# Kernel optimization log

Hardware: AMD Instinct MI355X
Metric: run time of the kernel (lower is better)

The kernel has to match this reference:

```python
import jax, jax.numpy as jnp
import numpy as np

# HalfKA_v2 canonical constants
FT_INPUT_DIM = 45056
FT_OUTPUT_DIM = 1024
PSQT_BUCKETS = 8
LAYER_STACKS = 8
FC0_OUT = 16
L2 = 15
FC1_IN_PAD = 32
FC1_OUT = 32
FC2_IN_PAD = 32
B = 8192
FEATS = 32  # active features per sample


def round_ste(x):
    # forward: round; backward: identity (straight-through)
    return x + jax.lax.stop_gradient(jnp.round(x) - x)


def fake_quant(w, bits):
    qmax = (1 << (bits - 1)) - 1
    return jnp.clip(round_ste(w), -qmax - 1, qmax)


def sparse_sum(w, feats, offsets, nb):
    # EmbeddingBag(mode='sum'): gather rows and segment-sum per sample.
    gathered = w[feats]                               # [total_feats, D]
    n = feats.shape[0]
    sid = jnp.zeros((n,), jnp.int32).at[offsets[1:]].set(1).cumsum()
    return jax.ops.segment_sum(gathered, sid, num_segments=nb)


def setup_inputs() -> dict:
    key = jax.random.key(0)
    ks = jax.random.split(key, 8)
    w_feats = jax.random.randint(ks[0], (B * FEATS,), 0, FT_INPUT_DIM)
    b_feats = jax.random.randint(ks[1], (B * FEATS,), 0, FT_INPUT_DIM)
    offs = jnp.arange(B, dtype=jnp.int32) * FEATS
    stm = jax.random.randint(ks[2], (B,), 0, 2)
    bucket = jax.random.randint(ks[3], (B,), 0, LAYER_STACKS)
    ft_weight = jax.random.normal(ks[4], (FT_INPUT_DIM, FT_OUTPUT_DIM), jnp.float32) * 5.0
    ft_bias = jnp.full((FT_OUTPUT_DIM,), 30.0, jnp.float32)
    psqt_weight = jnp.zeros((FT_INPUT_DIM, PSQT_BUCKETS), jnp.float32)
    fc0_w = jax.random.normal(ks[5], (LAYER_STACKS, FC0_OUT, FT_OUTPUT_DIM), jnp.float32) * 3.0
    fc0_b = jnp.zeros((LAYER_STACKS, FC0_OUT), jnp.float32)
    fc1_w = jax.random.normal(ks[6], (LAYER_STACKS, FC1_OUT, FC1_IN_PAD), jnp.float32) * 3.0
    fc1_b = jnp.zeros((LAYER_STACKS, FC1_OUT), jnp.float32)
    fc2_w = jax.random.normal(ks[7], (LAYER_STACKS, 1, FC2_IN_PAD), jnp.float32) * 3.0
    fc2_b = jnp.zeros((LAYER_STACKS, 1), jnp.float32)
    return dict(w_feats=w_feats, w_offsets=offs, b_feats=b_feats, b_offsets=offs,
                stm=stm, bucket=bucket, ft_weight=ft_weight, ft_bias=ft_bias,
                psqt_weight=psqt_weight, fc0_w=fc0_w, fc0_b=fc0_b,
                fc1_w=fc1_w, fc1_b=fc1_b, fc2_w=fc2_w, fc2_b=fc2_b)


def reference(w_feats, w_offsets, b_feats, b_offsets, stm, bucket,
              ft_weight, ft_bias, psqt_weight,
              fc0_w, fc0_b, fc1_w, fc1_b, fc2_w, fc2_b):
    nb = stm.shape[0]
    ftw = fake_quant(ft_weight, 16)
    ftb = fake_quant(ft_bias, 16)
    psq = fake_quant(psqt_weight, 32)

    acc_w = sparse_sum(ftw, w_feats, w_offsets, nb) + ftb
    acc_b = sparse_sum(ftw, b_feats, b_offsets, nb) + ftb
    psqt_w = sparse_sum(psq, w_feats, w_offsets, nb)
    psqt_b = sparse_sum(psq, b_feats, b_offsets, nb)

    stm_f = stm.astype(ft_weight.dtype)[:, None]
    acc_stm = acc_w * (1 - stm_f) + acc_b * stm_f
    acc_opp = acc_b * (1 - stm_f) + acc_w * stm_f

    H = FT_OUTPUT_DIM // 2

    def pairwise(a):
        return jnp.clip(a[:, :H], 0.0, 127.0) * jnp.clip(a[:, H:], 0.0, 127.0) / 128.0

    ft = jnp.concatenate([pairwise(acc_stm), pairwise(acc_opp)], axis=-1)  # [B, 1024]

    fc0w = fake_quant(fc0_w, 8); fc0b = fake_quant(fc0_b, 32)
    fc1w = fake_quant(fc1_w, 8); fc1b = fake_quant(fc1_b, 32)
    fc2w = fake_quant(fc2_w, 8); fc2b = fake_quant(fc2_b, 32)

    bsel3 = bucket[:, None, None]
    # fc0: compute all 8 tiny stacks, then select per-sample bucket (equivalent to mask routing)
    o0_all = jnp.einsum('bf,sof->bso', ft, fc0w) + fc0b[None]      # [B, S, 16]
    o0 = jnp.take_along_axis(o0_all, bsel3, axis=1)[:, 0]           # [B, 16]

    sqr = jnp.clip(o0[:, :L2] ** 2 / float(1 << 19), 0.0, 127.0)
    rel = jnp.clip(o0[:, :L2] / float(1 << 6), 0.0, 127.0)
    slab = jnp.concatenate([sqr, rel, jnp.zeros((nb, FC1_IN_PAD - 2 * L2), ft.dtype)], axis=-1)

    o1_all = jnp.einsum('bi,soi->bso', slab, fc1w) + fc1b[None]     # [B, S, 32]
    o1 = jnp.take_along_axis(o1_all, bsel3, axis=1)[:, 0]
    ac1 = jnp.clip(o1 / float(1 << 6), 0.0, 127.0)

    o2_all = jnp.einsum('bi,soi->bso', ac1, fc2w) + fc2b[None]      # [B, S, 1]
    scalar = jnp.take_along_axis(o2_all, bsel3, axis=1)[:, 0]       # [B, 1]

    skip = o0[:, 15:16] * (9600.0 / 8128.0)
    positional = scalar + skip

    psqt_stm = psqt_w * (1 - stm_f) + psqt_b * stm_f
    psqt_opp = psqt_b * (1 - stm_f) + psqt_w * stm_f
    bsel = bucket[:, None]
    psqt_v = (jnp.take_along_axis(psqt_stm, bsel, axis=1)
              - jnp.take_along_axis(psqt_opp, bsel, axis=1)) / 2.0

    return ((psqt_v + positional)[:, 0]) / 16.0
```

## Files before the change

kernel.cpp:

```cpp
#include <hip/hip_runtime.h>


#define NFEATS 32
#define FT_OUT 1024
#define HALF   512
#define NC4    256
#define TBL_BYTES  (45056u * 1024u)
#define TBL_N4     11534336
#define FC0Q_BYTES (8u * 16u * 1024u * 4u)

typedef short v2s __attribute__((ext_vector_type(2)));

__device__ __forceinline__ float q16f(float x) {
    float r = rintf(x);
    return fminf(fmaxf(r, -32768.f), 32767.f);
}
__device__ __forceinline__ float q8f(float x) {
    float r = rintf(x);
    return fminf(fmaxf(r, -128.f), 127.f);
}
__device__ __forceinline__ float4 q8f4(float4 v) {
    return make_float4(q8f(v.x), q8f(v.y), q8f(v.z), q8f(v.w));
}
__device__ __forceinline__ float clip127(float x) {
    return fminf(fmaxf(x, 0.f), 127.f);
}

__device__ __forceinline__ v2s sx_even(int p) {
    union { int i; v2s s; } u; u.i = p << 8; u.s = u.s >> 8; return u.s;
}
__device__ __forceinline__ v2s sx_odd(int p) {
    union { int i; v2s s; } u; u.i = p; u.s = u.s >> 8; return u.s;
}

__device__ __forceinline__ int pack4i8(float4 v) {
    const int a = (int)rintf(fminf(fmaxf(v.x, -127.f), 127.f));
    const int b = (int)rintf(fminf(fmaxf(v.y, -127.f), 127.f));
    const int c = (int)rintf(fminf(fmaxf(v.z, -127.f), 127.f));
    const int d = (int)rintf(fminf(fmaxf(v.w, -127.f), 127.f));
    return (a & 0xff) | ((b & 0xff) << 8) | ((c & 0xff) << 16) | (d << 24);
}

__global__ __launch_bounds__(256) void cvt_all(
    const float4* __restrict__ tbl, int* __restrict__ tbl_o,
    const float4* __restrict__ fc0, float4* __restrict__ fc0_o,
    int tbl_n4, int fc0_n4)
{
    const int i = blockIdx.x * 256 + threadIdx.x;
    if (i < tbl_n4) {
        tbl_o[i] = pack4i8(tbl[i]);
    } else {
        const int j = i - tbl_n4;
        if (j < fc0_n4) fc0_o[j] = q8f4(fc0[j]);
    }
}

template <int MODE>
__global__ __launch_bounds__(256) void nnue_v2(
    const int* __restrict__ w_feats, const int* __restrict__ w_offsets,
    const int* __restrict__ b_feats, const int* __restrict__ b_offsets,
    const int* __restrict__ stm_arr, const int* __restrict__ bucket_arr,
    const float* __restrict__ ft_weight, const char* __restrict__ ft_i8,
    const float* __restrict__ ft_bias,
    const float* __restrict__ psqt_weight,
    const float* __restrict__ fc0_w, const float* __restrict__ wq0,
    const float* __restrict__ fc0_b,
    const float* __restrict__ fc1_w, const float* __restrict__ fc1_b,
    const float* __restrict__ fc2_w, const float* __restrict__ fc2_b,
    float* __restrict__ out,
    int n_wf, int n_bf, int nb)
{
    const int b = blockIdx.x;
    const int t = threadIdx.x;
    const int l = t & 63;
    const int w = t >> 6;

    __shared__ int   s_fw[NFEATS], s_fb[NFEATS];
    __shared__ v2s   s_part[2][4][512];
    __shared__ float s_stm[FT_OUT];
    __shared__ float s_opp[FT_OUT];
    __shared__ float s_ft[FT_OUT];
    __shared__ float s_o0[16];
    __shared__ float s_slab[32];
    __shared__ float s_ac1[32];
    __shared__ float s_psqt[2];

    const int ws = w_offsets[b];
    const int we = (b + 1 < nb) ? w_offsets[b + 1] : n_wf;
    const int bs = b_offsets[b];
    const int be = (b + 1 < nb) ? b_offsets[b + 1] : n_bf;
    const int cw = min(we - ws, NFEATS);
    const int cb = min(be - bs, NFEATS);

    if (t < NFEATS) {
        s_fw[t] = (t < cw) ? w_feats[ws + t] : 0;
    } else if (t < 2 * NFEATS) {
        const int k = t - NFEATS;
        s_fb[k] = (k < cb) ? b_feats[bs + k] : 0;
    }
    __syncthreads();

    const int stm = stm_arr[b];
    const int bk  = bucket_arr[b];

    if (t < 64) {
        const int side = t >> 5;
        const int k    = t & 31;
        const int cnt  = side ? cb : cw;
        float v = 0.f;
        if (k < cnt) {
            const int f = side ? s_fb[k] : s_fw[k];
            v = rintf(psqt_weight[f * 8 + bk]);
        }
        v += __shfl_down(v, 16, 32);
        v += __shfl_down(v,  8, 32);
        v += __shfl_down(v,  4, 32);
        v += __shfl_down(v,  2, 32);
        v += __shfl_down(v,  1, 32);
        if (k == 0) s_psqt[side] = v;
    }

    float4 fw4, fb4;

    if constexpr (MODE >= 1) {
        v2s eW[4] = {{0,0},{0,0},{0,0},{0,0}}, oW[4] = {{0,0},{0,0},{0,0},{0,0}};
        v2s eB[4] = {{0,0},{0,0},{0,0},{0,0}}, oB[4] = {{0,0},{0,0},{0,0},{0,0}};
        const char* bp = ft_i8 + (size_t)(l * 16);

        if (cw == NFEATS && cb == NFEATS) {
            #pragma unroll
            for (int i = 0; i < 8; ++i) {
                const int k = w + 4 * i;
                const int4 p = *(const int4*)(bp + (size_t)s_fw[k] * 1024);
                const int4 q = *(const int4*)(bp + (size_t)s_fb[k] * 1024);
                eW[0] += sx_even(p.x); oW[0] += sx_odd(p.x);
                eW[1] += sx_even(p.y); oW[1] += sx_odd(p.y);
                eW[2] += sx_even(p.z); oW[2] += sx_odd(p.z);
                eW[3] += sx_even(p.w); oW[3] += sx_odd(p.w);
                eB[0] += sx_even(q.x); oB[0] += sx_odd(q.x);
                eB[1] += sx_even(q.y); oB[1] += sx_odd(q.y);
                eB[2] += sx_even(q.z); oB[2] += sx_odd(q.z);
                eB[3] += sx_even(q.w); oB[3] += sx_odd(q.w);
            }
        } else {
            for (int k = w; k < cw; k += 4) {
                const int4 p = *(const int4*)(bp + (size_t)s_fw[k] * 1024);
                eW[0] += sx_even(p.x); oW[0] += sx_odd(p.x);
                eW[1] += sx_even(p.y); oW[1] += sx_odd(p.y);
                eW[2] += sx_even(p.z); oW[2] += sx_odd(p.z);
                eW[3] += sx_even(p.w); oW[3] += sx_odd(p.w);
            }
            for (int k = w; k < cb; k += 4) {
                const int4 q = *(const int4*)(bp + (size_t)s_fb[k] * 1024);
                eB[0] += sx_even(q.x); oB[0] += sx_odd(q.x);
                eB[1] += sx_even(q.y); oB[1] += sx_odd(q.y);
                eB[2] += sx_even(q.z); oB[2] += sx_odd(q.z);
                eB[3] += sx_even(q.w); oB[3] += sx_odd(q.w);
            }
        }

        #pragma unroll
        for (int d = 0; d < 4; ++d) {
            s_part[0][w][d * 128 + 2 * l    ] = eW[d];
            s_part[0][w][d * 128 + 2 * l + 1] = oW[d];
            s_part[1][w][d * 128 + 2 * l    ] = eB[d];
            s_part[1][w][d * 128 + 2 * l + 1] = oB[d];
        }
        __syncthreads();

        const int ri = (t & 3) * 128 + 2 * (t >> 2);
        v2s ew = s_part[0][0][ri];     ew += s_part[0][1][ri];
        ew += s_part[0][2][ri];        ew += s_part[0][3][ri];
        v2s ow = s_part[0][0][ri + 1]; ow += s_part[0][1][ri + 1];
        ow += s_part[0][2][ri + 1];    ow += s_part[0][3][ri + 1];
        v2s eb = s_part[1][0][ri];     eb += s_part[1][1][ri];
        eb += s_part[1][2][ri];        eb += s_part[1][3][ri];
        v2s ob = s_part[1][0][ri + 1]; ob += s_part[1][1][ri + 1];
        ob += s_part[1][2][ri + 1];    ob += s_part[1][3][ri + 1];
        fw4 = make_float4((float)ew.x, (float)ow.x, (float)ew.y, (float)ow.y);
        fb4 = make_float4((float)eb.x, (float)ob.x, (float)eb.y, (float)ob.y);
    } else {
        const float4* ftw4 = reinterpret_cast<const float4*>(ft_weight);
        float4 aw = make_float4(0.f, 0.f, 0.f, 0.f);
        float4 ab = make_float4(0.f, 0.f, 0.f, 0.f);
        for (int k = 0; k < cw; ++k) {
            const float4 v = ftw4[s_fw[k] * NC4 + t];
            aw.x += rintf(v.x); aw.y += rintf(v.y);
            aw.z += rintf(v.z); aw.w += rintf(v.w);
        }
        for (int k = 0; k < cb; ++k) {
            const float4 u = ftw4[s_fb[k] * NC4 + t];
            ab.x += rintf(u.x); ab.y += rintf(u.y);
            ab.z += rintf(u.z); ab.w += rintf(u.w);
        }
        fw4 = aw; fb4 = ab;
    }

    {
        const float4 bv = reinterpret_cast<const float4*>(ft_bias)[t];
        const float bx = q16f(bv.x), by = q16f(bv.y), bz = q16f(bv.z), bw = q16f(bv.w);
        fw4.x += bx; fw4.y += by; fw4.z += bz; fw4.w += bw;
        fb4.x += bx; fb4.y += by; fb4.z += bz; fb4.w += bw;
    }

    reinterpret_cast<float4*>(s_stm)[t] = stm ? fb4 : fw4;
    reinterpret_cast<float4*>(s_opp)[t] = stm ? fw4 : fb4;
    __syncthreads();

    {
        float4 lo, hi;
        if (t < 128) {
            lo = reinterpret_cast<const float4*>(s_stm)[t];
            hi = reinterpret_cast<const float4*>(s_stm)[t + 128];
        } else {
            lo = reinterpret_cast<const float4*>(s_opp)[t - 128];
            hi = reinterpret_cast<const float4*>(s_opp)[t];
        }
        float4 r;
        r.x = clip127(lo.x) * clip127(hi.x) * 0.0078125f;
        r.y = clip127(lo.y) * clip127(hi.y) * 0.0078125f;
        r.z = clip127(lo.z) * clip127(hi.z) * 0.0078125f;
        r.w = clip127(lo.w) * clip127(hi.w) * 0.0078125f;
        reinterpret_cast<float4*>(s_ft)[t] = r;
    }
    __syncthreads();

    {
        const float4* ftf4 = reinterpret_cast<const float4*>(s_ft);
        const float4 f0 = ftf4[l], f1 = ftf4[l + 64],
                     f2 = ftf4[l + 128], f3 = ftf4[l + 192];
        const float4* wbase = (MODE == 2)
            ? reinterpret_cast<const float4*>(wq0)
            : reinterpret_cast<const float4*>(fc0_w);
        #pragma unroll
        for (int o = 0; o < 4; ++o) {
            const int orow = 4 * w + o;
            const float4* wr = wbase + ((size_t)bk * 16 + orow) * NC4;
            float4 w0 = wr[l], w1 = wr[l + 64], w2 = wr[l + 128], w3 = wr[l + 192];
            if constexpr (MODE != 2) {
                w0 = q8f4(w0); w1 = q8f4(w1); w2 = q8f4(w2); w3 = q8f4(w3);
            }
            float acc = f0.x * w0.x + f0.y * w0.y + f0.z * w0.z + f0.w * w0.w
                      + f1.x * w1.x + f1.y * w1.y + f1.z * w1.z + f1.w * w1.w
                      + f2.x * w2.x + f2.y * w2.y + f2.z * w2.z + f2.w * w2.w
                      + f3.x * w3.x + f3.y * w3.y + f3.z * w3.z + f3.w * w3.w;
            acc += __shfl_down(acc, 32);
            acc += __shfl_down(acc, 16);
            acc += __shfl_down(acc,  8);
            acc += __shfl_down(acc,  4);
            acc += __shfl_down(acc,  2);
            acc += __shfl_down(acc,  1);
            if (l == 0) s_o0[orow] = acc + rintf(fc0_b[bk * 16 + orow]);
        }
    }
    __syncthreads();

    if (t < 32) {
        float v;
        if (t < 15) {
            const float x = s_o0[t];
            v = clip127(x * x * (1.f / 524288.f));
        } else if (t < 30) {
            v = clip127(s_o0[t - 15] * 0.015625f);
        } else {
            v = 0.f;
        }
        s_slab[t] = v;
    }
    __syncthreads();

    if (t < 32) {
        const float* w1 = fc1_w + (size_t)bk * 32 * 32 + t * 32;
        float acc = rintf(fc1_b[bk * 32 + t]);
        #pragma unroll
        for (int i = 0; i < 32; ++i)
            acc += s_slab[i] * q8f(w1[i]);
        s_ac1[t] = clip127(acc * 0.015625f);
    }
    __syncthreads();

    if (t == 0) {
        const float* w2 = fc2_w + (size_t)bk * 32;
        float acc = rintf(fc2_b[bk]);
        #pragma unroll
        for (int i = 0; i < 32; ++i)
            acc += s_ac1[i] * q8f(w2[i]);
        const float skip = s_o0[15] * (float)(9600.0 / 8128.0);
        const float ps   = stm ? s_psqt[1] : s_psqt[0];
        const float po   = stm ? s_psqt[0] : s_psqt[1];
        out[b] = (0.5f * (ps - po) + acc + skip) * 0.0625f;
    }
}

extern "C" void kernel_launch(void* const* d_in, const int* in_sizes, int n_in,
                              void* d_out, int out_size, void* d_ws, size_t ws_size,
                              hipStream_t stream) {
    const int*   w_feats   = (const int*)d_in[0];
    const int*   w_offsets = (const int*)d_in[1];
    const int*   b_feats   = (const int*)d_in[2];
    const int*   b_offsets = (const int*)d_in[3];
    const int*   stm       = (const int*)d_in[4];
    const int*   bucket    = (const int*)d_in[5];
    const float* ft_weight = (const float*)d_in[6];
    const float* ft_bias   = (const float*)d_in[7];
    const float* psqt_w    = (const float*)d_in[8];
    const float* fc0_w     = (const float*)d_in[9];
    const float* fc0_b     = (const float*)d_in[10];
    const float* fc1_w     = (const float*)d_in[11];
    const float* fc1_b     = (const float*)d_in[12];
    const float* fc2_w     = (const float*)d_in[13];
    const float* fc2_b     = (const float*)d_in[14];
    float*       out       = (float*)d_out;

    const int nb   = in_sizes[4];
    const int n_wf = in_sizes[0];
    const int n_bf = in_sizes[2];

    const bool has_i8 = ws_size >= TBL_BYTES;
    const bool has_wq = ws_size >= TBL_BYTES + FC0Q_BYTES;
    float* wq0 = (float*)((char*)d_ws + TBL_BYTES);

    if (has_i8) {
        const int fc0_n4 = has_wq ? 32768 : 0;
        const int nblk = (TBL_N4 + fc0_n4 + 255) / 256;
        cvt_all<<<nblk, 256, 0, stream>>>(
            (const float4*)ft_weight, (int*)d_ws,
            (const float4*)fc0_w, (float4*)wq0, TBL_N4, fc0_n4);
        if (has_wq) {
            nnue_v2<2><<<nb, 256, 0, stream>>>(
                w_feats, w_offsets, b_feats, b_offsets, stm, bucket,
                ft_weight, (const char*)d_ws, ft_bias, psqt_w,
                fc0_w, wq0, fc0_b, fc1_w, fc1_b, fc2_w, fc2_b,
                out, n_wf, n_bf, nb);
        } else {
            nnue_v2<1><<<nb, 256, 0, stream>>>(
                w_feats, w_offsets, b_feats, b_offsets, stm, bucket,
                ft_weight, (const char*)d_ws, ft_bias, psqt_w,
                fc0_w, nullptr, fc0_b, fc1_w, fc1_b, fc2_w, fc2_b,
                out, n_wf, n_bf, nb);
        }
    } else {
        nnue_v2<0><<<nb, 256, 0, stream>>>(
            w_feats, w_offsets, b_feats, b_offsets, stm, bucket,
            ft_weight, nullptr, ft_bias, psqt_w,
            fc0_w, nullptr, fc0_b, fc1_w, fc1_b, fc2_w, fc2_b,
            out, n_wf, n_bf, nb);
    }
}
```

Measured before the change: 391.2 us.

## Split feature-transformer gather by side and drop cross-wave partial reduction

The sparse gather changes so each half of the block (128 threads) handles one perspective: every thread reads 8 bytes per row across all 32 features, instead of four waves each taking a quarter of the features and reducing partials through shared memory. This removes the s_part shared buffer, one barrier and the reduction pass, and shrinks LDS use. In exchange each thread issues more serial dependent loads. The conversion kernel now packs 8 float4s per thread, and the fc1 and fc2 weights are also pre-quantized into the workspace.

```diff
diff --git a/kernel.cpp b/kernel.cpp
--- a/kernel.cpp
+++ b/kernel.cpp
@@ -3,11 +3,14 @@
 
 #define NFEATS 32
 #define FT_OUT 1024
-#define HALF   512
 #define NC4    256
 #define TBL_BYTES  (45056u * 1024u)
 #define TBL_N4     11534336
-#define FC0Q_BYTES (8u * 16u * 1024u * 4u)
+#define TBL_G8     (TBL_N4 / 8)
+#define FC0_N4     32768
+#define FC1_N4     2048
+#define FC2_N4     64
+#define WQ_BYTES   ((FC0_N4 + FC1_N4 + FC2_N4) * 16u)
 
 typedef short v2s __attribute__((ext_vector_type(2)));
 
@@ -25,7 +28,6 @@
 __device__ __forceinline__ float clip127(float x) {
     return fminf(fmaxf(x, 0.f), 127.f);
 }
-
 __device__ __forceinline__ v2s sx_even(int p) {
     union { int i; v2s s; } u; u.i = p << 8; u.s = u.s >> 8; return u.s;
 }
@@ -41,29 +43,41 @@
     return (a & 0xff) | ((b & 0xff) << 8) | ((c & 0xff) << 16) | (d << 24);
 }
 
-__global__ __launch_bounds__(256) void cvt_all(
-    const float4* __restrict__ tbl, int* __restrict__ tbl_o,
-    const float4* __restrict__ fc0, float4* __restrict__ fc0_o,
-    int tbl_n4, int fc0_n4)
+__global__ __launch_bounds__(256) void cvt_v3(
+    const float4* __restrict__ tbl, int4* __restrict__ tbl_o,
+    const float4* __restrict__ fc0, const float4* __restrict__ fc1,
+    const float4* __restrict__ fc2, float4* __restrict__ wq,
+    int do_fc)
 {
     const int i = blockIdx.x * 256 + threadIdx.x;
-    if (i < tbl_n4) {
-        tbl_o[i] = pack4i8(tbl[i]);
-    } else {
-        const int j = i - tbl_n4;
-        if (j < fc0_n4) fc0_o[j] = q8f4(fc0[j]);
+    if (i < TBL_G8) {
+        const float4* p = tbl + (size_t)i * 8;
+        int4 a, b;
+        a.x = pack4i8(p[0]); a.y = pack4i8(p[1]);
+        a.z = pack4i8(p[2]); a.w = pack4i8(p[3]);
+        b.x = pack4i8(p[4]); b.y = pack4i8(p[5]);
+        b.z = pack4i8(p[6]); b.w = pack4i8(p[7]);
+        tbl_o[2 * (size_t)i]     = a;
+        tbl_o[2 * (size_t)i + 1] = b;
+    } else if (do_fc) {
+        int j = i - TBL_G8;
+        if (j < FC0_N4) { wq[j] = q8f4(fc0[j]); return; }
+        j -= FC0_N4;
+        if (j < FC1_N4) { wq[FC0_N4 + j] = q8f4(fc1[j]); return; }
+        j -= FC1_N4;
+        if (j < FC2_N4) { wq[FC0_N4 + FC1_N4 + j] = q8f4(fc2[j]); }
     }
 }
 
 template <int MODE>
-__global__ __launch_bounds__(256) void nnue_v2(
+__global__ __launch_bounds__(256) void nnue_v3(
     const int* __restrict__ w_feats, const int* __restrict__ w_offsets,
     const int* __restrict__ b_feats, const int* __restrict__ b_offsets,
     const int* __restrict__ stm_arr, const int* __restrict__ bucket_arr,
     const float* __restrict__ ft_weight, const char* __restrict__ ft_i8,
     const float* __restrict__ ft_bias,
     const float* __restrict__ psqt_weight,
-    const float* __restrict__ fc0_w, const float* __restrict__ wq0,
+    const float* __restrict__ fc0_w, const float* __restrict__ wq,
     const float* __restrict__ fc0_b,
     const float* __restrict__ fc1_w, const float* __restrict__ fc1_b,
     const float* __restrict__ fc2_w, const float* __restrict__ fc2_b,
@@ -75,11 +89,9 @@
     const int l = t & 63;
     const int w = t >> 6;
 
-    __shared__ int   s_fw[NFEATS], s_fb[NFEATS];
-    __shared__ v2s   s_part[2][4][512];
-    __shared__ float s_stm[FT_OUT];
-    __shared__ float s_opp[FT_OUT];
-    __shared__ float s_ft[FT_OUT];
+    __shared__ int s_fw[NFEATS], s_fb[NFEATS];
+    __shared__ __align__(16) float s_acc[2][FT_OUT];
+    __shared__ __align__(16) float s_ft[FT_OUT];
     __shared__ float s_o0[16];
     __shared__ float s_slab[32];
     __shared__ float s_ac1[32];
@@ -120,65 +132,38 @@
         if (k == 0) s_psqt[side] = v;
     }
 
-    float4 fw4, fb4;
-
     if constexpr (MODE >= 1) {
-        v2s eW[4] = {{0,0},{0,0},{0,0},{0,0}}, oW[4] = {{0,0},{0,0},{0,0},{0,0}};
-        v2s eB[4] = {{0,0},{0,0},{0,0},{0,0}}, oB[4] = {{0,0},{0,0},{0,0},{0,0}};
-        const char* bp = ft_i8 + (size_t)(l * 16);
-
+        const int side = t >> 7;
+        const int u    = t & 127;
+        const int* rows = side ? s_fb : s_fw;
+        const int  cnt  = side ? cb : cw;
+        const char* bp = ft_i8 + (size_t)(u * 8);
+
+        v2s e0 = {0,0}, o0 = {0,0}, e1 = {0,0}, o1 = {0,0};
         if (cw == NFEATS && cb == NFEATS) {
-            #pragma unroll
-            for (int i = 0; i < 8; ++i) {
-                const int k = w + 4 * i;
-                const int4 p = *(const int4*)(bp + (size_t)s_fw[k] * 1024);
-                const int4 q = *(const int4*)(bp + (size_t)s_fb[k] * 1024);
-                eW[0] += sx_even(p.x); oW[0] += sx_odd(p.x);
-                eW[1] += sx_even(p.y); oW[1] += sx_odd(p.y);
-                eW[2] += sx_even(p.z); oW[2] += sx_odd(p.z);
-                eW[3] += sx_even(p.w); oW[3] += sx_odd(p.w);
-                eB[0] += sx_even(q.x); oB[0] += sx_odd(q.x);
-                eB[1] += sx_even(q.y); oB[1] += sx_odd(q.y);
-                eB[2] += sx_even(q.z); oB[2] += sx_odd(q.z);
-                eB[3] += sx_even(q.w); oB[3] += sx_odd(q.w);
+            #pragma unroll 8
+            for (int k = 0; k < NFEATS; ++k) {
+                const int2 p = *(const int2*)(bp + (size_t)rows[k] * 1024);
+                e0 += sx_even(p.x); o0 += sx_odd(p.x);
+                e1 += sx_even(p.y); o1 += sx_odd(p.y);
             }
         } else {
-            for (int k = w; k < cw; k += 4) {
-                const int4 p = *(const int4*)(bp + (size_t)s_fw[k] * 1024);
-                eW[0] += sx_even(p.x); oW[0] += sx_odd(p.x);
-                eW[1] += sx_even(p.y); oW[1] += sx_odd(p.y);
-                eW[2] += sx_even(p.z); oW[2] += sx_odd(p.z);
-                eW[3] += sx_even(p.w); oW[3] += sx_odd(p.w);
+            for (int k = 0; k < cnt; ++k) {
+                const int2 p = *(const int2*)(bp + (size_t)rows[k] * 1024);
+                e0 += sx_even(p.x); o0 += sx_odd(p.x);
+                e1 += sx_even(p.y); o1 += sx_odd(p.y);
             }
-            for (int k = w; k < cb; k += 4) {
-                const int4 q = *(const int4*)(bp + (size_t)s_fb[k] * 1024);
-                eB[0] += sx_even(q.x); oB[0] += sx_odd(q.x);
-                eB[1] += sx_even(q.y); oB[1] += sx_odd(q.y);
-                eB[2] += sx_even(q.z); oB[2] += sx_odd(q.z);
-                eB[3] += sx_even(q.w); oB[3] += sx_odd(q.w);
-            }
-        }
-
-        #pragma unroll
-        for (int d = 0; d < 4; ++d) {
-            s_part[0][w][d * 128 + 2 * l    ] = eW[d];
-            s_part[0][w][d * 128 + 2 * l + 1] = oW[d];
-            s_part[1][w][d * 128 + 2 * l    ] = eB[d];
-            s_part[1][w][d * 128 + 2 * l + 1] = oB[d];
-        }
-        __syncthreads();
-
-        const int ri = (t & 3) * 128 + 2 * (t >> 2);
-        v2s ew = s_part[0][0][ri];     ew += s_part[0][1][ri];
-        ew += s_part[0][2][ri];        ew += s_part[0][3][ri];
-        v2s ow = s_part[0][0][ri + 1]; ow += s_part[0][1][ri + 1];
-        ow += s_part[0][2][ri + 1];    ow += s_part[0][3][ri + 1];
-        v2s eb = s_part[1][0][ri];     eb += s_part[1][1][ri];
-        eb += s_part[1][2][ri];        eb += s_part[1][3][ri];
-        v2s ob = s_part[1][0][ri + 1]; ob += s_part[1][1][ri + 1];
-        ob += s_part[1][2][ri + 1];    ob += s_part[1][3][ri + 1];
-        fw4 = make_float4((float)ew.x, (float)ow.x, (float)ew.y, (float)ow.y);
-        fb4 = make_float4((float)eb.x, (float)ob.x, (float)eb.y, (float)ob.y);
+        }
+
+        const float4 b0 = reinterpret_cast<const float4*>(ft_bias)[2 * u];
+        const float4 b1 = reinterpret_cast<const float4*>(ft_bias)[2 * u + 1];
+        float4 r0, r1;
+        r0.x = (float)e0.x + q16f(b0.x); r0.y = (float)o0.x + q16f(b0.y);
+        r0.z = (float)e0.y + q16f(b0.z); r0.w = (float)o0.y + q16f(b0.w);
+        r1.x = (float)e1.x + q16f(b1.x); r1.y = (float)o1.x + q16f(b1.y);
+        r1.z = (float)e1.y + q16f(b1.z); r1.w = (float)o1.y + q16f(b1.w);
+        reinterpret_cast<float4*>(&s_acc[side][8 * u])[0] = r0;
+        reinterpret_cast<float4*>(&s_acc[side][8 * u])[1] = r1;
     } else {
         const float4* ftw4 = reinterpret_cast<const float4*>(ft_weight);
         float4 aw = make_float4(0.f, 0.f, 0.f, 0.f);
@@ -189,32 +174,29 @@
             aw.z += rintf(v.z); aw.w += rintf(v.w);
         }
         for (int k = 0; k < cb; ++k) {
-            const float4 u = ftw4[s_fb[k] * NC4 + t];
-            ab.x += rintf(u.x); ab.y += rintf(u.y);
-            ab.z += rintf(u.z); ab.w += rintf(u.w);
-        }
-        fw4 = aw; fb4 = ab;
-    }
-
-    {
+            const float4 u4 = ftw4[s_fb[k] * NC4 + t];
+            ab.x += rintf(u4.x); ab.y += rintf(u4.y);
+            ab.z += rintf(u4.z); ab.w += rintf(u4.w);
+        }
         const float4 bv = reinterpret_cast<const float4*>(ft_bias)[t];
         const float bx = q16f(bv.x), by = q16f(bv.y), bz = q16f(bv.z), bw = q16f(bv.w);
-        fw4.x += bx; fw4.y += by; fw4.z += bz; fw4.w += bw;
-        fb4.x += bx; fb4.y += by; fb4.z += bz; fb4.w += bw;
-    }
-
-    reinterpret_cast<float4*>(s_stm)[t] = stm ? fb4 : fw4;
-    reinterpret_cast<float4*>(s_opp)[t] = stm ? fw4 : fb4;
+        aw.x += bx; aw.y += by; aw.z += bz; aw.w += bw;
+        ab.x += bx; ab.y += by; ab.z += bz; ab.w += bw;
+        reinterpret_cast<float4*>(&s_acc[0][4 * t])[0] = aw;
+        reinterpret_cast<float4*>(&s_acc[1][4 * t])[0] = ab;
+    }
     __syncthreads();
 
     {
         float4 lo, hi;
         if (t < 128) {
-            lo = reinterpret_cast<const float4*>(s_stm)[t];
-            hi = reinterpret_cast<const float4*>(s_stm)[t + 128];
+            const float* sp = s_acc[stm];
+            lo = reinterpret_cast<const float4*>(sp)[t];
+            hi = reinterpret_cast<const float4*>(sp)[t + 128];
         } else {
-            lo = reinterpret_cast<const float4*>(s_opp)[t - 128];
-            hi = reinterpret_cast<const float4*>(s_opp)[t];
+            const float* sp = s_acc[1 - stm];
+            lo = reinterpret_cast<const float4*>(sp)[t - 128];
+            hi = reinterpret_cast<const float4*>(sp)[t];
         }
         float4 r;
         r.x = clip127(lo.x) * clip127(hi.x) * 0.0078125f;
@@ -230,7 +212,7 @@
         const float4 f0 = ftf4[l], f1 = ftf4[l + 64],
                      f2 = ftf4[l + 128], f3 = ftf4[l + 192];
         const float4* wbase = (MODE == 2)
-            ? reinterpret_cast<const float4*>(wq0)
+            ? reinterpret_cast<const float4*>(wq)
             : reinterpret_cast<const float4*>(fc0_w);
         #pragma unroll
         for (int o = 0; o < 4; ++o) {
@@ -270,21 +252,29 @@
     __syncthreads();
 
     if (t < 32) {
-        const float* w1 = fc1_w + (size_t)bk * 32 * 32 + t * 32;
+        const float* w1 = (MODE == 2)
+            ? wq + FC0_N4 * 4 + (size_t)bk * 32 * 32 + t * 32
+            : fc1_w + (size_t)bk * 32 * 32 + t * 32;
         float acc = rintf(fc1_b[bk * 32 + t]);
         #pragma unroll
-        for (int i = 0; i < 32; ++i)
-            acc += s_slab[i] * q8f(w1[i]);
+        for (int i = 0; i < 32; ++i) {
+            const float wv = (MODE == 2) ? w1[i] : q8f(w1[i]);
+            acc += s_slab[i] * wv;
+        }
         s_ac1[t] = clip127(acc * 0.015625f);
     }
     __syncthreads();
 
     if (t == 0) {
-        const float* w2 = fc2_w + (size_t)bk * 32;
+        const float* w2 = (MODE == 2)
+            ? wq + (FC0_N4 + FC1_N4) * 4 + (size_t)bk * 32
+            : fc2_w + (size_t)bk * 32;
         float acc = rintf(fc2_b[bk]);
         #pragma unroll
-        for (int i = 0; i < 32; ++i)
-            acc += s_ac1[i] * q8f(w2[i]);
+        for (int i = 0; i < 32; ++i) {
+            const float wv = (MODE == 2) ? w2[i] : q8f(w2[i]);
+            acc += s_ac1[i] * wv;
+        }
         const float skip = s_o0[15] * (float)(9600.0 / 8128.0);
         const float ps   = stm ? s_psqt[1] : s_psqt[0];
         const float po   = stm ? s_psqt[0] : s_psqt[1];
@@ -317,30 +307,30 @@
     const int n_bf = in_sizes[2];
 
     const bool has_i8 = ws_size >= TBL_BYTES;
-    const bool has_wq = ws_size >= TBL_BYTES + FC0Q_BYTES;
-    float* wq0 = (float*)((char*)d_ws + TBL_BYTES);
+    const bool has_wq = ws_size >= TBL_BYTES + WQ_BYTES;
+    float* wq = (float*)((char*)d_ws + TBL_BYTES);
 
     if (has_i8) {
-        const int fc0_n4 = has_wq ? 32768 : 0;
-        const int nblk = (TBL_N4 + fc0_n4 + 255) / 256;
-        cvt_all<<<nblk, 256, 0, stream>>>(
-            (const float4*)ft_weight, (int*)d_ws,
-            (const float4*)fc0_w, (float4*)wq0, TBL_N4, fc0_n4);
+        const int nthreads = TBL_G8 + (has_wq ? (FC0_N4 + FC1_N4 + FC2_N4) : 0);
+        cvt_v3<<<(nthreads + 255) / 256, 256, 0, stream>>>(
+            (const float4*)ft_weight, (int4*)d_ws,
+            (const float4*)fc0_w, (const float4*)fc1_w, (const float4*)fc2_w,
+            (float4*)wq, has_wq ? 1 : 0);
         if (has_wq) {
-            nnue_v2<2><<<nb, 256, 0, stream>>>(
+            nnue_v3<2><<<nb, 256, 0, stream>>>(
                 w_feats, w_offsets, b_feats, b_offsets, stm, bucket,
                 ft_weight, (const char*)d_ws, ft_bias, psqt_w,
-                fc0_w, wq0, fc0_b, fc1_w, fc1_b, fc2_w, fc2_b,
+                fc0_w, wq, fc0_b, fc1_w, fc1_b, fc2_w, fc2_b,
                 out, n_wf, n_bf, nb);
         } else {
-            nnue_v2<1><<<nb, 256, 0, stream>>>(
+            nnue_v3<1><<<nb, 256, 0, stream>>>(
                 w_feats, w_offsets, b_feats, b_offsets, stm, bucket,
                 ft_weight, (const char*)d_ws, ft_bias, psqt_w,
                 fc0_w, nullptr, fc0_b, fc1_w, fc1_b, fc2_w, fc2_b,
                 out, n_wf, n_bf, nb);
         }
     } else {
-        nnue_v2<0><<<nb, 256, 0, stream>>>(
+        nnue_v3<0><<<nb, 256, 0, stream>>>(
             w_feats, w_offsets, b_feats, b_offsets, stm, bucket,
             ft_weight, nullptr, ft_bias, psqt_w,
             fc0_w, nullptr, fc0_b, fc1_w, fc1_b, fc2_w, fc2_b,
```

Result: faster. 366.7 us (-6.3%).
